# Kernel optimization log

Hardware: AMD Instinct MI355X
Metric: run time of the kernel (lower is better)

The kernel has to match this reference:

```python
import jax, jax.numpy as jnp
import numpy as np

DT = 0.001
TAU_SYN_INV = 200.0  # norse default 1/5e-3
TAU_MEM_INV = 100.0  # norse default 1/1e-2
V_TH = 0.4
ALPHA = 10.0  # SuperSpike surrogate slope


@jax.custom_vjp
def heaviside(x):
    # SuperSpike: heaviside forward, 1/(alpha*|x|+1)^2 surrogate backward
    return (x > 0).astype(x.dtype)

def _h_fwd(x):
    return heaviside(x), x

def _h_bwd(x, g):
    return (g / (ALPHA * jnp.abs(x) + 1.0) ** 2,)

heaviside.defvjp(_h_fwd, _h_bwd)


def conv(x, w, b, stride=1):
    y = jax.lax.conv_general_dilated(
        x, w, (stride, stride), 'VALID',
        dimension_numbers=('NCHW', 'OIHW', 'NCHW'))
    return y + b[None, :, None, None]


def maxpool2(x):
    return jax.lax.reduce_window(x, -jnp.inf, jax.lax.max, (1, 1, 2, 2), (1, 1, 2, 2), 'VALID')


def setup_inputs() -> dict:
    key = jax.random.key(0)
    ks = jax.random.split(key, 11)
    B, T, H, W = 32, 64, 64, 64
    num_classes = 10
    F = 96 * 12 * 12  # flattened encoder size = 13824
    HID = 128

    def u(k, shape, fan_in):
        bound = 1.0 / np.sqrt(fan_in)
        return jax.random.uniform(k, shape, jnp.float32, -bound, bound)

    return dict(
        x=jax.random.normal(ks[0], (B, T, 1, H, W), jnp.float32),
        w1=u(ks[1], (32, 1, 5, 5), 25), b1=u(ks[2], (32,), 25),
        w2=u(ks[3], (64, 32, 3, 3), 32 * 9), b2=u(ks[4], (64,), 32 * 9),
        w3=u(ks[5], (96, 64, 3, 3), 64 * 9), b3=u(ks[6], (96,), 64 * 9),
        w_in=jax.random.normal(ks[7], (HID, F), jnp.float32) / np.sqrt(F),
        w_rec=jax.random.normal(ks[8], (HID, HID), jnp.float32) / np.sqrt(HID),
        w_fc=u(ks[9], (num_classes, HID), HID),
        b_fc=u(ks[10], (num_classes,), HID),
    )


def reference(x, w1, b1, w2, b2, w3, b3, w_in, w_rec, w_fc, b_fc):
    B, T = x.shape[0], x.shape[1]
    HID = w_in.shape[0]
    C = w_fc.shape[0]

    # encoder vectorized over all B*T frames
    frames = x.reshape(B * T, x.shape[2], x.shape[3], x.shape[4])
    z = jax.nn.relu(conv(frames, w1, b1, stride=2))  # [BT,32,30,30]
    z = jax.nn.relu(conv(z, w2, b2))                 # [BT,64,28,28]
    z = maxpool2(z)                                  # [BT,64,14,14]
    z = jax.nn.relu(conv(z, w3, b3))                 # [BT,96,12,12]
    feats = z.reshape(B, T, -1)                      # [B,T,13824]

    # precompute feed-forward input currents for all timesteps
    ff = jnp.einsum('btf,hf->tbh', feats, w_in)      # [T,B,HID]

    def step(carry, ff_t):
        z_p, v, i, vr, ir = carry
        # LIF recurrent cell (norse lif_step, v_leak=0, v_reset=0)
        v_dec = v + DT * TAU_MEM_INV * (-v + i)
        i_dec = i - DT * TAU_SYN_INV * i
        z_n = heaviside(v_dec - V_TH)
        v_n = (1.0 - z_n) * v_dec
        i_n = i_dec + ff_t + z_p @ w_rec.T  # recurrent uses previous spikes
        # readout linear + LI cell (norse li_feed_forward_step)
        ro = z_n @ w_fc.T + b_fc
        vr_n = vr + DT * TAU_MEM_INV * (-vr + ir)
        ir_n = ir - DT * TAU_SYN_INV * ir + ro
        return (z_n, v_n, i_n, vr_n, ir_n), vr_n

    zeros_h = jnp.zeros((B, HID), x.dtype)
    zeros_c = jnp.zeros((B, C), x.dtype)
    carry0 = (zeros_h, zeros_h, zeros_h, zeros_c, zeros_c)
    _, voltages = jax.lax.scan(step, carry0, ff)     # [T,B,C]

    out = jnp.max(voltages, axis=0)                  # [B,C]
    return jax.nn.log_softmax(out, axis=1)
```

## Files before the change

### kernel.cpp

```cpp
#include <hip/hip_runtime.h>
#include <math.h>

typedef _Float16 half8 __attribute__((ext_vector_type(8)));
typedef _Float16 half4 __attribute__((ext_vector_type(4)));
typedef float f32x16 __attribute__((ext_vector_type(16)));

__global__ __launch_bounds__(256) void xprep_k(const float* __restrict__ x,
                                               _Float16* __restrict__ xh,
                                               _Float16* __restrict__ xl) {
  const int i = blockIdx.x * 256 + threadIdx.x;
  if (i >= 2097152) return;
  const float4 v = *(const float4*)(x + (size_t)i * 4);
  half4 h, l;
  const float vv[4] = {v.x, v.y, v.z, v.w};
#pragma unroll
  for (int e = 0; e < 4; ++e) {
    const _Float16 hh = (_Float16)vv[e];
    h[e] = hh;
    l[e] = (_Float16)((vv[e] - (float)hh) * 1024.0f);
  }
  *(half4*)(xh + (size_t)i * 4) = h;
  *(half4*)(xl + (size_t)i * 4) = l;
}

__global__ __launch_bounds__(256) void w1prep_k(const float* __restrict__ w1,
                                                _Float16* __restrict__ w1p) {
  const int i = blockIdx.x * 256 + threadIdx.x;
  if (i >= 1024) return;
  const int blk = i >> 8;
  const int s = blk >> 1, g = blk & 1;
  const int ch = (i >> 3) & 31, e = i & 7;
  const int k = s * 16 + g * 8 + e;
  float v = 0.f;
  if (k < 25) v = w1[ch * 25 + k];
  const _Float16 h = (_Float16)v;
  w1p[i] = h;
  w1p[1024 + i] = (_Float16)((v - (float)h) * 1024.0f);
}

__global__ __launch_bounds__(256) void w2prep_k(const float* __restrict__ w2,
                                                _Float16* __restrict__ w2p) {
  const int i = blockIdx.x * 256 + threadIdx.x;
  if (i >= 18432) return;
  const int tap = i >> 11;
  const int r = i & 2047;
  const int blk = r >> 8;
  const int nt = blk >> 2, s = (blk >> 1) & 1, g = blk & 1;
  const int n = (r >> 3) & 31, e = r & 7;
  const int och = nt * 32 + n;
  const int ic = s * 16 + g * 8 + e;
  const float v = w2[och * 288 + ic * 9 + tap];
  const _Float16 h = (_Float16)v;
  const _Float16 l = (_Float16)((v - (float)h) * 1024.0f);
  w2p[i] = h;
  w2p[18432 + i] = l;
}

__global__ __launch_bounds__(256) void w3prep_k(const float* __restrict__ w3,
                                                _Float16* __restrict__ w3p) {
  const int i = blockIdx.x * 256 + threadIdx.x;
  if (i >= 55296) return;
  const int icc = i / 27648;
  const int r1 = i - icc * 27648;
  const int tc = r1 / 6144;
  const int rem = r1 - tc * 6144;
  const int tl = rem / 3072;
  const int rem2 = rem - tl * 3072;
  const int nt = rem2 >> 10;
  const int s = (rem2 >> 9) & 1;
  const int g = (rem2 >> 8) & 1;
  const int n = (rem2 >> 3) & 31;
  const int e = rem2 & 7;
  const int tap = tc * 2 + tl;
  const int och = nt * 32 + n;
  const int ic = icc * 32 + s * 16 + g * 8 + e;
  const float v = w3[(size_t)och * 576 + ic * 9 + tap];
  const _Float16 h = (_Float16)v;
  const _Float16 l = (_Float16)((v - (float)h) * 1024.0f);
  w3p[i] = h;
  w3p[55296 + i] = l;
}

__global__ __launch_bounds__(256) void winprep_k(const float* __restrict__ w_in,
                                                 _Float16* __restrict__ winp) {
  const int i = blockIdx.x * 256 + threadIdx.x;
  if (i >= 1769472) return;
  const int ks = i >> 11;
  const int rem = i & 2047;
  const int nt = rem >> 9;
  const int g = (rem >> 8) & 1;
  const int n = (rem >> 3) & 31;
  const int e = rem & 7;
  const int h = nt * 32 + n;
  const int k = ks * 16 + g * 8 + e;
  const float v = w_in[(size_t)h * 13824 + k];
  const _Float16 hh = (_Float16)v;
  const _Float16 ll = (_Float16)((v - (float)hh) * 1024.0f);
  winp[i] = hh;
  winp[1769472 + i] = ll;
}

__global__ __launch_bounds__(448) void conv2f_mfma_k(
    const _Float16* __restrict__ xh, const _Float16* __restrict__ xl,
    const float* __restrict__ b1, const _Float16* __restrict__ w1p,
    const _Float16* __restrict__ w2p, const float* __restrict__ b2,
    _Float16* __restrict__ y2s) {
  __shared__ __align__(16) _Float16 S[30464];
  const int rp = blockIdx.x;
  const int img0 = blockIdx.y * 2;
  const int tid = threadIdx.x;

  for (int i = tid; i < 480; i += 448) {
    const int plane = i / 240;
    const int r2 = i - plane * 240;
    const int j = r2 / 120;
    const int c8 = r2 - j * 120;
    const _Float16* src = (plane ? xl : xh) + (size_t)(img0 + j) * 4096 +
                          rp * 512 + c8 * 8;
    *(float4*)&S[23040 + plane * 1920 + j * 960 + c8 * 8] =
        *(const float4*)src;
  }
  __syncthreads();

  const int w = tid >> 6;
  const int lane = tid & 63;
  const int l31 = lane & 31;
  const int g = lane >> 5;

  {
    const float b1c = b1[l31];
    const int gb = l31 >> 3, e0 = l31 & 7;
    int xoffs[16];
#pragma unroll
    for (int s = 0; s < 2; ++s)
#pragma unroll
      for (int e = 0; e < 8; ++e) {
        const int k = s * 16 + g * 8 + e;
        const int ky = k / 5, kx = k - (k / 5) * 5;
        xoffs[s * 8 + e] = (k < 25) ? (ky * 64 + kx) : -1;
      }
#pragma unroll 1
    for (int ti = 0; ti < 2; ++ti) {
      const int t = w + ti * 7;
      if (t >= 12) break;
      const int p = t * 32 + l31;
      const int pcl = (p < 360) ? p : 359;
      const int img = pcl / 180;
      const int rem = pcl - img * 180;
      const int row = rem / 30;
      const int col = rem - row * 30;
      const int xb = img * 960 + (2 * row) * 64 + 2 * col;
      f32x16 acc_h = {}, acc_l = {};
#pragma unroll
      for (int s = 0; s < 2; ++s) {
        half8 ah, al;
#pragma unroll
        for (int e = 0; e < 8; ++e) {
          const int o = xoffs[s * 8 + e];
          _Float16 hv = (_Float16)0.f, lv = (_Float16)0.f;
          if (o >= 0) {
            hv = S[23040 + xb + o];
            lv = S[24960 + xb + o];
          }
          ah[e] = hv;
          al[e] = lv;
        }
        const _Float16* bp = w1p + ((s * 2 + g) * 32 + l31) * 8;
        half8 bh = *(const half8*)bp;
        half8 bl = *(const half8*)(bp + 1024);
        acc_h = __builtin_amdgcn_mfma_f32_32x32x16_f16(ah, bh, acc_h, 0, 0, 0);
        acc_l = __builtin_amdgcn_mfma_f32_32x32x16_f16(ah, bl, acc_l, 0, 0, 0);
        acc_l = __builtin_amdgcn_mfma_f32_32x32x16_f16(al, bh, acc_l, 0, 0, 0);
      }
#pragma unroll
      for (int r = 0; r < 16; ++r) {
        const int mrow = (r & 3) + 8 * (r >> 2) + 4 * g;
        const int pp = t * 32 + mrow;
        if (pp < 360) {
          const int im = pp / 180;
          const int rm = pp - im * 180;
          const int cl = rm - (rm / 30) * 30;
          const int swz = (cl >> 1) & 3;
          const int addr = im * 5760 + rm * 32 + ((gb ^ swz) << 3) + e0;
          const float val =
              fmaxf(acc_h[r] + acc_l[r] * 9.765625e-4f + b1c, 0.f);
          const _Float16 hh = (_Float16)val;
          S[addr] = hh;
          S[11520 + addr] = (_Float16)((val - (float)hh) * 1024.0f);
        }
      }
    }
  }
  __syncthreads();

  const int m = w * 32 + l31;
  const int aimg = m / 112;
  const int apos = m - aimg * 112;
  const int ar = apos / 28;
  const int ax = apos - ar * 28;
  const int icg = g * 8;

  f32x16 acc00 = {}, acc01 = {}, acc10 = {}, acc11 = {};

  const _Float16* bb = w2p + g * 256 + l31 * 8;
  half8 pbh0, pbl0, pbh1, pbl1;
  half8 qbh0, qbl0, qbh1, qbl1;
  {
    pbh0 = *(const half8*)&bb[0];
    pbl0 = *(const half8*)&bb[18432];
    pbh1 = *(const half8*)&bb[1024];
    pbl1 = *(const half8*)&bb[18432 + 1024];
  }
#pragma unroll 1
  for (int i = 0; i < 18; i += 2) {
    {
      const int tap = (i + 1) >> 1, s = (i + 1) & 1;
      const _Float16* bt = bb + tap * 2048 + s * 512;
      qbh0 = *(const half8*)&bt[0];
      qbl0 = *(const half8*)&bt[18432];
      qbh1 = *(const half8*)&bt[1024];
      qbl1 = *(const half8*)&bt[18432 + 1024];
    }
    {
      const int tap = i >> 1, s = i & 1;
      const int ky = tap / 3, kx = tap - (tap / 3) * 3;
      const int acol = ax + kx;
      const int swzA = ((acol >> 1) & 3) << 3;
      const int abase = aimg * 5760 + ((ar + ky) * 30 + acol) * 32;
      const int icoA = (s * 16 + icg) ^ swzA;
      half8 ah = *(const half8*)&S[abase + icoA];
      half8 al = *(const half8*)&S[11520 + abase + icoA];
      acc00 = __builtin_amdgcn_mfma_f32_32x32x16_f16(ah, pbh0, acc00, 0, 0, 0);
      acc10 = __builtin_amdgcn_mfma_f32_32x32x16_f16(ah, pbl0, acc10, 0, 0, 0);
      acc10 = __builtin_amdgcn_mfma_f32_32x32x16_f16(al, pbh0, acc10, 0, 0, 0);
      acc01 = __builtin_amdgcn_mfma_f32_32x32x16_f16(ah, pbh1, acc01, 0, 0, 0);
      acc11 = __builtin_amdgcn_mfma_f32_32x32x16_f16(ah, pbl1, acc11, 0, 0, 0);
      acc11 = __builtin_amdgcn_mfma_f32_32x32x16_f16(al, pbh1, acc11, 0, 0, 0);
    }
    if (i + 2 < 18) {
      const int tap = (i + 2) >> 1, s = (i + 2) & 1;
      const _Float16* bt = bb + tap * 2048 + s * 512;
      pbh0 = *(const half8*)&bt[0];
      pbl0 = *(const half8*)&bt[18432];
      pbh1 = *(const half8*)&bt[1024];
      pbl1 = *(const half8*)&bt[18432 + 1024];
    }
    {
      const int ii = i + 1;
      const int tap = ii >> 1, s = ii & 1;
      const int ky = tap / 3, kx = tap - (tap / 3) * 3;
      const int acol = ax + kx;
      const int swzA = ((acol >> 1) & 3) << 3;
      const int abase = aimg * 5760 + ((ar + ky) * 30 + acol) * 32;
      const int icoA = (s * 16 + icg) ^ swzA;
      half8 ah = *(const half8*)&S[abase + icoA];
      half8 al = *(const half8*)&S[11520 + abase + icoA];
      acc00 = __builtin_amdgcn_mfma_f32_32x32x16_f16(ah, qbh0, acc00, 0, 0, 0);
      acc10 = __builtin_amdgcn_mfma_f32_32x32x16_f16(ah, qbl0, acc10, 0, 0, 0);
      acc10 = __builtin_amdgcn_mfma_f32_32x32x16_f16(al, qbh0, acc10, 0, 0, 0);
      acc01 = __builtin_amdgcn_mfma_f32_32x32x16_f16(ah, qbh1, acc01, 0, 0, 0);
      acc11 = __builtin_amdgcn_mfma_f32_32x32x16_f16(ah, qbl1, acc11, 0, 0, 0);
      acc11 = __builtin_amdgcn_mfma_f32_32x32x16_f16(al, qbh1, acc11, 0, 0, 0);
    }
  }
  __syncthreads();
  float* sPool = (float*)S;
#pragma unroll
  for (int r = 0; r < 16; ++r) {
    const int mrow = (r & 3) + 8 * (r >> 2) + 4 * g;
    const int mo = w * 32 + mrow;
    sPool[mo * 68 + l31] = acc00[r] + acc10[r] * 9.765625e-4f;
    sPool[mo * 68 + 32 + l31] = acc01[r] + acc11[r] * 9.765625e-4f;
  }
  __syncthreads();
  {
    const int img = tid / 224;
    const int r1 = tid - img * 224;
    const int pr = r1 / 112;
    const int r2 = r1 - pr * 112;
    const int pc = r2 >> 3;
    const int blk = r2 & 7;
    const int m00 = img * 112 + pr * 56 + pc * 2;
    const float* s0 = &sPool[m00 * 68 + blk * 8];
    float rowv[4][8];
    *(float4*)&rowv[0][0] = *(const float4*)s0;
    *(float4*)&rowv[0][4] = *(const float4*)(s0 + 4);
    *(float4*)&rowv[1][0] = *(const float4*)(s0 + 68);
    *(float4*)&rowv[1][4] = *(const float4*)(s0 + 72);
    *(float4*)&rowv[2][0] = *(const float4*)(s0 + 28 * 68);
    *(float4*)&rowv[2][4] = *(const float4*)(s0 + 28 * 68 + 4);
    *(float4*)&rowv[3][0] = *(const float4*)(s0 + 29 * 68);
    *(float4*)&rowv[3][4] = *(const float4*)(s0 + 29 * 68 + 4);
    half8 hv, lv;
#pragma unroll
    for (int e = 0; e < 8; ++e) {
      const float mx =
          fmaxf(fmaxf(rowv[0][e], rowv[1][e]), fmaxf(rowv[2][e], rowv[3][e]));
      const float val = fmaxf(mx + b2[blk * 8 + e], 0.f);
      const _Float16 hh = (_Float16)val;
      hv[e] = hh;
      lv[e] = (_Float16)((val - (float)hh) * 1024.0f);
    }
    const int posg = (rp * 2 + pr) * 14 + pc;
    const int icc = blk >> 2;
    const int slot = (blk & 3) ^ ((posg >> 1) & 3);
    _Float16* dh =
        y2s + (size_t)(img0 + img) * 25088 + icc * 6272 + posg * 32 + slot * 8;
    *(float4*)dh = *(float4*)&hv;
    *(float4*)(dh + 12544) = *(float4*)&lv;
  }
}

__global__ __launch_bounds__(320) void conv3_mfma_k(
    const _Float16* __restrict__ y2s, const _Float16* __restrict__ w3p,
    const float* __restrict__ b3, _Float16* __restrict__ fh,
    _Float16* __restrict__ fl) {
  __shared__ __align__(16) _Float16 S[12544];
  const int img = blockIdx.x;
  const int tid = threadIdx.x;
  const int w = tid >> 6;
  const int lane = tid & 63;
  const int l31 = lane & 31;
  const int g = lane >> 5;
  const int m = w * 32 + l31;
  const int mc = (m < 144) ? m : 143;
  const int r = mc / 12, c = mc - (mc / 12) * 12;

  f32x16 acch[3] = {};
  f32x16 accl[3] = {};

  const _Float16* bb = w3p + g * 256 + l31 * 8;
#pragma unroll 1
  for (int icc = 0; icc < 2; ++icc) {
    __syncthreads();
    {
      const _Float16* src = y2s + (size_t)img * 25088 + icc * 6272;
      for (int c8 = tid; c8 < 784; c8 += 320) {
        *(float4*)&S[c8 * 8] = *(const float4*)&src[c8 * 8];
        *(float4*)&S[6272 + c8 * 8] = *(const float4*)&src[12544 + c8 * 8];
      }
    }
    __syncthreads();
#pragma unroll 1
    for (int tc = 0; tc < 5; ++tc) {
      const int ntaps = (tc == 4) ? 1 : 2;
#pragma unroll 1
      for (int tl = 0; tl < ntaps; ++tl) {
        const int tap = tc * 2 + tl;
        const int ky = tap / 3, kx = tap - (tap / 3) * 3;
        const int pix = (r + ky) * 14 + (c + kx);
        const int pswz = (pix >> 1) & 3;
        half8 ah[2], al[2];
#pragma unroll
        for (int s = 0; s < 2; ++s) {
          const int o = pix * 32 + ((s * 2 + g) ^ pswz) * 8;
          ah[s] = *(const half8*)&S[o];
          al[s] = *(const half8*)&S[6272 + o];
        }
        const _Float16* bt = bb + icc * 27648 + tc * 6144 + tl * 3072;
#pragma unroll
        for (int nt = 0; nt < 3; ++nt) {
#pragma unroll
          for (int s = 0; s < 2; ++s) {
            const _Float16* bp = bt + nt * 1024 + s * 512;
            half8 bh = *(const half8*)bp;
            half8 bl = *(const half8*)(bp + 55296);
            acch[nt] =
                __builtin_amdgcn_mfma_f32_32x32x16_f16(ah[s], bh, acch[nt], 0, 0, 0);
            accl[nt] =
                __builtin_amdgcn_mfma_f32_32x32x16_f16(ah[s], bl, accl[nt], 0, 0, 0);
            accl[nt] =
                __builtin_amdgcn_mfma_f32_32x32x16_f16(al[s], bh, accl[nt], 0, 0, 0);
          }
        }
      }
    }
  }
  float* sO = (float*)S;
#pragma unroll
  for (int nt = 0; nt < 3; ++nt) {
    __syncthreads();
#pragma unroll
    for (int rr = 0; rr < 16; ++rr) {
      const int row = (rr & 3) + 8 * (rr >> 2) + 4 * g;
      const int pos = w * 32 + row;
      if (pos < 144)
        sO[l31 * 145 + pos] = acch[nt][rr] + accl[nt][rr] * 9.765625e-4f;
    }
    __syncthreads();
    for (int idx8 = tid; idx8 < 576; idx8 += 320) {
      const int oc = idx8 / 18;
      const int pb = idx8 - oc * 18;
      const float bb2 = b3[nt * 32 + oc];
      half8 hv, lv;
#pragma unroll
      for (int e = 0; e < 8; ++e) {
        const float v = fmaxf(sO[oc * 145 + pb * 8 + e] + bb2, 0.f);
        const _Float16 hh = (_Float16)v;
        hv[e] = hh;
        lv[e] = (_Float16)((v - (float)hh) * 1024.0f);
      }
      const size_t ko = (size_t)img * 13824 + (nt * 32 + oc) * 144 + pb * 8;
      *(float4*)&fh[ko] = *(float4*)&hv;
      *(float4*)&fl[ko] = *(float4*)&lv;
    }
  }
}

__global__ __launch_bounds__(256) void ffgemm_k(
    const _Float16* __restrict__ fh, const _Float16* __restrict__ fl,
    const _Float16* __restrict__ winp, float* __restrict__ P, int frame0,
    int Cl) {
  __shared__ __align__(16) _Float16 S[24576];
  const int mb = blockIdx.x;
  const int kc = blockIdx.y;
  const int tid = threadIdx.x;
  const int w = tid >> 6;
  const int lane = tid & 63;
  const int l31 = lane & 31;
  const int g = lane >> 5;
  const int mt = w >> 1;
  const int nt0 = (w & 1) * 2;
  f32x16 acc_h[2] = {};
  f32x16 acc_l[2] = {};
  const int kbase = kc * 1728;
#pragma unroll 1
  for (int kt = 0; kt < 27; ++kt) {
    __syncthreads();
    for (int i = tid; i < 512; i += 256) {
      const int row = i >> 3, kb = i & 7;
      int rc = mb * 64 + row;
      if (rc >= Cl) rc = Cl - 1;
      const size_t so = (size_t)rc * 13824 + kbase + kt * 64 + kb * 8;
      const int d = row * 64 + ((kb ^ (row & 7)) * 8);
      *(float4*)&S[d] = *(const float4*)&fh[so];
      *(float4*)&S[4096 + d] = *(const float4*)&fl[so];
    }
    {
      const size_t bo = (size_t)(kc * 108 + kt * 4) * 2048;
      for (int i = tid; i < 1024; i += 256) {
        *(float4*)&S[8192 + i * 8] = *(const float4*)&winp[bo + i * 8];
        *(float4*)&S[16384 + i * 8] =
            *(const float4*)&winp[1769472 + bo + i * 8];
      }
    }
    __syncthreads();
#pragma unroll
    for (int ks = 0; ks < 4; ++ks) {
      const int kb = ks * 2 + g;
      const int ao = (mt * 32 + l31) * 64 + ((kb ^ (l31 & 7)) * 8);
      half8 ah = *(const half8*)&S[ao];
      half8 al = *(const half8*)&S[4096 + ao];
#pragma unroll
      for (int j = 0; j < 2; ++j) {
        const int nt = nt0 + j;
        const int b = 8192 + (((ks * 4 + nt) * 2 + g) * 32 + l31) * 8;
        half8 bh = *(const half8*)&S[b];
        half8 bl = *(const half8*)&S[8192 + b];
        acc_h[j] = __builtin_amdgcn_mfma_f32_32x32x16_f16(ah, bh, acc_h[j], 0, 0, 0);
        acc_l[j] = __builtin_amdgcn_mfma_f32_32x32x16_f16(ah, bl, acc_l[j], 0, 0, 0);
        acc_l[j] = __builtin_amdgcn_mfma_f32_32x32x16_f16(al, bh, acc_l[j], 0, 0, 0);
      }
    }
  }
  float* Pp = P + ((size_t)kc * 2048 + (size_t)frame0) * 128;
#pragma unroll
  for (int j = 0; j < 2; ++j) {
    const int h = (nt0 + j) * 32 + l31;
#pragma unroll
    for (int r = 0; r < 16; ++r) {
      const int row = (r & 3) + 8 * (r >> 2) + 4 * g;
      const int fr = mb * 64 + mt * 32 + row;
      if (fr < Cl)
        Pp[(size_t)fr * 128 + h] = acc_h[j][r] + acc_l[j][r] * 9.765625e-4f;
    }
  }
}

__global__ __launch_bounds__(256) void ffreduce_k(const float* __restrict__ P,
                                                  float* __restrict__ ffo) {
  const int i = blockIdx.x * 256 + threadIdx.x;
  float s = 0.f;
#pragma unroll
  for (int kcc = 0; kcc < 8; ++kcc) s += P[(size_t)kcc * 262144 + i];
  ffo[i] = s;
}

__global__ __launch_bounds__(64) void scan_k(
    const float* __restrict__ ff, const float* __restrict__ w_rec,
    const float* __restrict__ w_fc, const float* __restrict__ b_fc,
    float* __restrict__ out) {
#pragma clang fp contract(off)
  __shared__ float sWr[16384];
  const int b = blockIdx.x;
  const int t = threadIdx.x;
  for (int idx = t; idx < 16384; idx += 64) {
    int hh = idx >> 7, j = idx & 127;
    sWr[j * 128 + hh] = w_rec[idx];
  }
  float wf0[10], wf1[10], bf[10];
#pragma unroll
  for (int c = 0; c < 10; ++c) {
    wf0[c] = w_fc[c * 128 + t];
    wf1[c] = w_fc[c * 128 + 64 + t];
    bf[c] = b_fc[c];
  }
  __syncthreads();
  float v0 = 0.f, v1 = 0.f, i0 = 0.f, i1 = 0.f;
  float vr[10], ir[10], vmax[10];
#pragma unroll
  for (int c = 0; c < 10; ++c) {
    vr[c] = 0.f;
    ir[c] = 0.f;
    vmax[c] = -1e30f;
  }
  unsigned long long pm0 = 0ull, pm1 = 0ull;
  const float* ffb = ff + (size_t)b * 8192;
#pragma unroll 1
  for (int ts = 0; ts < 64; ++ts) {
    const float vd0 = v0 + 0.1f * (i0 - v0);
    const float vd1 = v1 + 0.1f * (i1 - v1);
    const float id0 = i0 - 0.2f * i0;
    const float id1 = i1 - 0.2f * i1;
    const bool z0 = (vd0 - 0.4f) > 0.f;
    const bool z1 = (vd1 - 0.4f) > 0.f;
    v0 = z0 ? 0.f : vd0;
    v1 = z1 ? 0.f : vd1;
    float rec0 = 0.f, rec1 = 0.f;
    unsigned long long mm = pm0;
    while (mm) {
      int j = __ffsll(mm) - 1;
      mm &= mm - 1;
      rec0 += sWr[j * 128 + t];
      rec1 += sWr[j * 128 + t + 64];
    }
    mm = pm1;
    while (mm) {
      int j = __ffsll(mm) - 1;
      mm &= mm - 1;
      rec0 += sWr[(j + 64) * 128 + t];
      rec1 += sWr[(j + 64) * 128 + t + 64];
    }
    i0 = (id0 + ffb[ts * 128 + t]) + rec0;
    i1 = (id1 + ffb[ts * 128 + 64 + t]) + rec1;
    pm0 = __ballot(z0);
    pm1 = __ballot(z1);
#pragma unroll
    for (int c = 0; c < 10; ++c) {
      float val = (z0 ? wf0[c] : 0.f) + (z1 ? wf1[c] : 0.f);
      val += __shfl_xor(val, 1);
      val += __shfl_xor(val, 2);
      val += __shfl_xor(val, 4);
      val += __shfl_xor(val, 8);
      val += __shfl_xor(val, 16);
      val += __shfl_xor(val, 32);
      const float ro = val + bf[c];
      vr[c] = vr[c] + 0.1f * (ir[c] - vr[c]);
      vmax[c] = fmaxf(vmax[c], vr[c]);
      ir[c] = (ir[c] - 0.2f * ir[c]) + ro;
    }
  }
  if (t == 0) {
    float M = vmax[0];
#pragma unroll
    for (int c = 1; c < 10; ++c) M = fmaxf(M, vmax[c]);
    float s = 0.f;
#pragma unroll
    for (int c = 0; c < 10; ++c) s += expf(vmax[c] - M);
    const float ls = logf(s);
#pragma unroll
    for (int c = 0; c < 10; ++c) out[b * 10 + c] = vmax[c] - M - ls;
  }
}

extern "C" void kernel_launch(void* const* d_in, const int* in_sizes, int n_in,
                              void* d_out, int out_size, void* d_ws,
                              size_t ws_size, hipStream_t stream) {
  (void)in_sizes;
  (void)n_in;
  (void)out_size;
  const float* x = (const float*)d_in[0];
  const float* w1 = (const float*)d_in[1];
  const float* b1 = (const float*)d_in[2];
  const float* w2 = (const float*)d_in[3];
  const float* b2 = (const float*)d_in[4];
  const float* w3 = (const float*)d_in[5];
  const float* b3 = (const float*)d_in[6];
  const float* w_in = (const float*)d_in[7];
  const float* w_rec = (const float*)d_in[8];
  const float* w_fc = (const float*)d_in[9];
  const float* b_fc = (const float*)d_in[10];
  float* out = (float*)d_out;
  char* ws = (char*)d_ws;

  const size_t OFF_W2P = 1048576ull + 8388608ull;
  const size_t OFF_W3P = OFF_W2P + 147456ull;
  const size_t OFF_WIN = OFF_W3P + 221184ull;
  const size_t OFF_W1P = OFF_WIN + 7077888ull;
  const size_t OFF_XH = OFF_W1P + 8192ull;
  const size_t OFF_XL = OFF_XH + 16777216ull;
  const size_t HDR = OFF_XL + 16777216ull;
  const size_t PERF = 50176ull + 55296ull;
  int C = 32;
  for (int c = 2048; c >= 32; c >>= 1) {
    if (HDR + (size_t)c * PERF <= ws_size) { C = c; break; }
  }
  float* ffbuf = (float*)ws;
  float* P = (float*)(ws + 1048576ull);
  _Float16* w2p = (_Float16*)(ws + OFF_W2P);
  _Float16* w3p = (_Float16*)(ws + OFF_W3P);
  _Float16* winp = (_Float16*)(ws + OFF_WIN);
  _Float16* w1p = (_Float16*)(ws + OFF_W1P);
  _Float16* xh = (_Float16*)(ws + OFF_XH);
  _Float16* xl = (_Float16*)(ws + OFF_XL);
  _Float16* y2s = (_Float16*)(ws + HDR);
  _Float16* fh = (_Float16*)(ws + HDR + (size_t)C * 50176ull);
  _Float16* fl = fh + (size_t)C * 13824;

  xprep_k<<<8192, 256, 0, stream>>>(x, xh, xl);
  w1prep_k<<<4, 256, 0, stream>>>(w1, w1p);
  w2prep_k<<<72, 256, 0, stream>>>(w2, w2p);
  w3prep_k<<<216, 256, 0, stream>>>(w3, w3p);
  winprep_k<<<6912, 256, 0, stream>>>(w_in, winp);

  const int nChunks = 2048 / C;
  const int mbN = (C + 63) / 64;
  for (int ch = 0; ch < nChunks; ++ch) {
    const int f0 = ch * C;
    conv2f_mfma_k<<<dim3(7, C / 2), 448, 0, stream>>>(
        xh + (size_t)f0 * 4096, xl + (size_t)f0 * 4096, b1, w1p, w2p, b2, y2s);
    conv3_mfma_k<<<C, 320, 0, stream>>>(y2s, w3p, b3, fh, fl);
    ffgemm_k<<<dim3(mbN, 8), 256, 0, stream>>>(fh, fl, winp, P, f0, C);
  }
  ffreduce_k<<<1024, 256, 0, stream>>>(P, ffbuf);
  scan_k<<<32, 64, 0, stream>>>(ffbuf, w_rec, w_fc, b_fc, out);
}
```

Before: 583.0 us.

## Process conv1 and pooling per image to shrink conv2 kernel shared memory

Conv1 input staging and compute in the fused conv1/conv2 kernel now run one image at a time instead of both at once. The pooling epilogue is likewise split into two passes, one per image, with a smaller pool buffer. Together these cut LDS from about 60KB to about 50KB per block, which may let more blocks share a CU. The cost is extra barriers, fewer active warps in the conv1 phase (6 of 7), and half the threads idle during each pooling pass.

```diff
diff --git a/kernel.cpp b/kernel.cpp
--- a/kernel.cpp
+++ b/kernel.cpp
@@ -105,22 +105,10 @@
     const float* __restrict__ b1, const _Float16* __restrict__ w1p,
     const _Float16* __restrict__ w2p, const float* __restrict__ b2,
     _Float16* __restrict__ y2s) {
-  __shared__ __align__(16) _Float16 S[30464];
+  __shared__ __align__(16) _Float16 S[24960];
   const int rp = blockIdx.x;
   const int img0 = blockIdx.y * 2;
   const int tid = threadIdx.x;
-
-  for (int i = tid; i < 480; i += 448) {
-    const int plane = i / 240;
-    const int r2 = i - plane * 240;
-    const int j = r2 / 120;
-    const int c8 = r2 - j * 120;
-    const _Float16* src = (plane ? xl : xh) + (size_t)(img0 + j) * 4096 +
-                          rp * 512 + c8 * 8;
-    *(float4*)&S[23040 + plane * 1920 + j * 960 + c8 * 8] =
-        *(const float4*)src;
-  }
-  __syncthreads();
 
   const int w = tid >> 6;
   const int lane = tid & 63;
@@ -140,58 +128,62 @@
         xoffs[s * 8 + e] = (k < 25) ? (ky * 64 + kx) : -1;
       }
 #pragma unroll 1
-    for (int ti = 0; ti < 2; ++ti) {
-      const int t = w + ti * 7;
-      if (t >= 12) break;
-      const int p = t * 32 + l31;
-      const int pcl = (p < 360) ? p : 359;
-      const int img = pcl / 180;
-      const int rem = pcl - img * 180;
-      const int row = rem / 30;
-      const int col = rem - row * 30;
-      const int xb = img * 960 + (2 * row) * 64 + 2 * col;
-      f32x16 acc_h = {}, acc_l = {};
-#pragma unroll
-      for (int s = 0; s < 2; ++s) {
-        half8 ah, al;
-#pragma unroll
-        for (int e = 0; e < 8; ++e) {
-          const int o = xoffs[s * 8 + e];
-          _Float16 hv = (_Float16)0.f, lv = (_Float16)0.f;
-          if (o >= 0) {
-            hv = S[23040 + xb + o];
-            lv = S[24960 + xb + o];
+    for (int ph = 0; ph < 2; ++ph) {
+      if (tid < 240) {
+        const int plane = tid / 120;
+        const int c8 = tid - plane * 120;
+        const _Float16* src = (plane ? xl : xh) +
+                              (size_t)(img0 + ph) * 4096 + rp * 512 + c8 * 8;
+        *(float4*)&S[23040 + plane * 960 + c8 * 8] = *(const float4*)src;
+      }
+      __syncthreads();
+      if (w < 6) {
+        const int p = w * 32 + l31;
+        const int pcl = (p < 180) ? p : 179;
+        const int row = pcl / 30;
+        const int col = pcl - row * 30;
+        const int xb = (2 * row) * 64 + 2 * col;
+        f32x16 acc_h = {}, acc_l = {};
+#pragma unroll
+        for (int s = 0; s < 2; ++s) {
+          half8 ah, al;
+#pragma unroll
+          for (int e = 0; e < 8; ++e) {
+            const int o = xoffs[s * 8 + e];
+            _Float16 hv = (_Float16)0.f, lv = (_Float16)0.f;
+            if (o >= 0) {
+              hv = S[23040 + xb + o];
+              lv = S[24000 + xb + o];
+            }
+            ah[e] = hv;
+            al[e] = lv;
           }
-          ah[e] = hv;
-          al[e] = lv;
+          const _Float16* bp = w1p + ((s * 2 + g) * 32 + l31) * 8;
+          half8 bh = *(const half8*)bp;
+          half8 bl = *(const half8*)(bp + 1024);
+          acc_h = __builtin_amdgcn_mfma_f32_32x32x16_f16(ah, bh, acc_h, 0, 0, 0);
+          acc_l = __builtin_amdgcn_mfma_f32_32x32x16_f16(ah, bl, acc_l, 0, 0, 0);
+          acc_l = __builtin_amdgcn_mfma_f32_32x32x16_f16(al, bh, acc_l, 0, 0, 0);
         }
-        const _Float16* bp = w1p + ((s * 2 + g) * 32 + l31) * 8;
-        half8 bh = *(const half8*)bp;
-        half8 bl = *(const half8*)(bp + 1024);
-        acc_h = __builtin_amdgcn_mfma_f32_32x32x16_f16(ah, bh, acc_h, 0, 0, 0);
-        acc_l = __builtin_amdgcn_mfma_f32_32x32x16_f16(ah, bl, acc_l, 0, 0, 0);
-        acc_l = __builtin_amdgcn_mfma_f32_32x32x16_f16(al, bh, acc_l, 0, 0, 0);
-      }
-#pragma unroll
-      for (int r = 0; r < 16; ++r) {
-        const int mrow = (r & 3) + 8 * (r >> 2) + 4 * g;
-        const int pp = t * 32 + mrow;
-        if (pp < 360) {
-          const int im = pp / 180;
-          const int rm = pp - im * 180;
-          const int cl = rm - (rm / 30) * 30;
-          const int swz = (cl >> 1) & 3;
-          const int addr = im * 5760 + rm * 32 + ((gb ^ swz) << 3) + e0;
-          const float val =
-              fmaxf(acc_h[r] + acc_l[r] * 9.765625e-4f + b1c, 0.f);
-          const _Float16 hh = (_Float16)val;
-          S[addr] = hh;
-          S[11520 + addr] = (_Float16)((val - (float)hh) * 1024.0f);
+#pragma unroll
+        for (int r = 0; r < 16; ++r) {
+          const int mrow = (r & 3) + 8 * (r >> 2) + 4 * g;
+          const int pp = w * 32 + mrow;
+          if (pp < 180) {
+            const int cl = pp - (pp / 30) * 30;
+            const int swz = (cl >> 1) & 3;
+            const int addr = ph * 5760 + pp * 32 + ((gb ^ swz) << 3) + e0;
+            const float val =
+                fmaxf(acc_h[r] + acc_l[r] * 9.765625e-4f + b1c, 0.f);
+            const _Float16 hh = (_Float16)val;
+            S[addr] = hh;
+            S[11520 + addr] = (_Float16)((val - (float)hh) * 1024.0f);
+          }
         }
       }
-    }
-  }
-  __syncthreads();
+      __syncthreads();
+    }
+  }
 
   const int m = w * 32 + l31;
   const int aimg = m / 112;
@@ -263,51 +255,56 @@
       acc11 = __builtin_amdgcn_mfma_f32_32x32x16_f16(al, qbh1, acc11, 0, 0, 0);
     }
   }
-  __syncthreads();
+
   float* sPool = (float*)S;
-#pragma unroll
-  for (int r = 0; r < 16; ++r) {
-    const int mrow = (r & 3) + 8 * (r >> 2) + 4 * g;
-    const int mo = w * 32 + mrow;
-    sPool[mo * 68 + l31] = acc00[r] + acc10[r] * 9.765625e-4f;
-    sPool[mo * 68 + 32 + l31] = acc01[r] + acc11[r] * 9.765625e-4f;
-  }
-  __syncthreads();
-  {
-    const int img = tid / 224;
-    const int r1 = tid - img * 224;
-    const int pr = r1 / 112;
-    const int r2 = r1 - pr * 112;
-    const int pc = r2 >> 3;
-    const int blk = r2 & 7;
-    const int m00 = img * 112 + pr * 56 + pc * 2;
-    const float* s0 = &sPool[m00 * 68 + blk * 8];
-    float rowv[4][8];
-    *(float4*)&rowv[0][0] = *(const float4*)s0;
-    *(float4*)&rowv[0][4] = *(const float4*)(s0 + 4);
-    *(float4*)&rowv[1][0] = *(const float4*)(s0 + 68);
-    *(float4*)&rowv[1][4] = *(const float4*)(s0 + 72);
-    *(float4*)&rowv[2][0] = *(const float4*)(s0 + 28 * 68);
-    *(float4*)&rowv[2][4] = *(const float4*)(s0 + 28 * 68 + 4);
-    *(float4*)&rowv[3][0] = *(const float4*)(s0 + 29 * 68);
-    *(float4*)&rowv[3][4] = *(const float4*)(s0 + 29 * 68 + 4);
-    half8 hv, lv;
-#pragma unroll
-    for (int e = 0; e < 8; ++e) {
-      const float mx =
-          fmaxf(fmaxf(rowv[0][e], rowv[1][e]), fmaxf(rowv[2][e], rowv[3][e]));
-      const float val = fmaxf(mx + b2[blk * 8 + e], 0.f);
-      const _Float16 hh = (_Float16)val;
-      hv[e] = hh;
-      lv[e] = (_Float16)((val - (float)hh) * 1024.0f);
-    }
-    const int posg = (rp * 2 + pr) * 14 + pc;
-    const int icc = blk >> 2;
-    const int slot = (blk & 3) ^ ((posg >> 1) & 3);
-    _Float16* dh =
-        y2s + (size_t)(img0 + img) * 25088 + icc * 6272 + posg * 32 + slot * 8;
-    *(float4*)dh = *(float4*)&hv;
-    *(float4*)(dh + 12544) = *(float4*)&lv;
+#pragma unroll 1
+  for (int ph = 0; ph < 2; ++ph) {
+    __syncthreads();
+#pragma unroll
+    for (int r = 0; r < 16; ++r) {
+      const int mrow = (r & 3) + 8 * (r >> 2) + 4 * g;
+      const int mo = w * 32 + mrow;
+      const int srow = mo - ph * 112;
+      if (srow >= 0 && srow < 112) {
+        sPool[srow * 68 + l31] = acc00[r] + acc10[r] * 9.765625e-4f;
+        sPool[srow * 68 + 32 + l31] = acc01[r] + acc11[r] * 9.765625e-4f;
+      }
+    }
+    __syncthreads();
+    if (tid < 224) {
+      const int pr = tid / 112;
+      const int r2 = tid - pr * 112;
+      const int pc = r2 >> 3;
+      const int blk = r2 & 7;
+      const int m00 = pr * 56 + pc * 2;
+      const float* s0 = &sPool[m00 * 68 + blk * 8];
+      float rowv[4][8];
+      *(float4*)&rowv[0][0] = *(const float4*)s0;
+      *(float4*)&rowv[0][4] = *(const float4*)(s0 + 4);
+      *(float4*)&rowv[1][0] = *(const float4*)(s0 + 68);
+      *(float4*)&rowv[1][4] = *(const float4*)(s0 + 72);
+      *(float4*)&rowv[2][0] = *(const float4*)(s0 + 28 * 68);
+      *(float4*)&rowv[2][4] = *(const float4*)(s0 + 28 * 68 + 4);
+      *(float4*)&rowv[3][0] = *(const float4*)(s0 + 29 * 68);
+      *(float4*)&rowv[3][4] = *(const float4*)(s0 + 29 * 68 + 4);
+      half8 hv, lv;
+#pragma unroll
+      for (int e = 0; e < 8; ++e) {
+        const float mx = fmaxf(fmaxf(rowv[0][e], rowv[1][e]),
+                               fmaxf(rowv[2][e], rowv[3][e]));
+        const float val = fmaxf(mx + b2[blk * 8 + e], 0.f);
+        const _Float16 hh = (_Float16)val;
+        hv[e] = hh;
+        lv[e] = (_Float16)((val - (float)hh) * 1024.0f);
+      }
+      const int posg = (rp * 2 + pr) * 14 + pc;
+      const int icc = blk >> 2;
+      const int slot = (blk & 3) ^ ((posg >> 1) & 3);
+      _Float16* dh = y2s + (size_t)(img0 + ph) * 25088 + icc * 6272 +
+                     posg * 32 + slot * 8;
+      *(float4*)dh = *(float4*)&hv;
+      *(float4*)(dh + 12544) = *(float4*)&lv;
+    }
   }
 }
 
```

After: 587.2 us. No clear change (+0.7%).
